# Optimization experiments

Hardware: AMD Instinct MI355X
Metric: run time of the kernel (lower is better)

The kernel has to match this reference:

```python
import jax, jax.numpy as jnp
import numpy as np

N_BANK = 1_000_000
D = 256
EPS = 1e-12  # torch F.normalize eps


def setup_inputs() -> dict:
    key = jax.random.key(0)
    k1, k2 = jax.random.split(key)
    query_emb = jax.random.normal(k1, (1, D), dtype=jnp.float32)
    emb_norm = jax.random.normal(k2, (N_BANK, D), dtype=jnp.float32)
    return {"query_emb": query_emb, "emb_norm": emb_norm, "k": 5}


def reference(query_emb, emb_norm, k):
    # L2-normalize query along feature dim (torch F.normalize semantics)
    norm = jnp.linalg.norm(query_emb, axis=1, keepdims=True)
    query = query_emb / jnp.maximum(norm, EPS)
    # [1, d] @ [d, N] -> [1, N] -> [N]
    sims = jnp.squeeze(query @ emb_norm.T, axis=0)
    top_vals, top_idx = jax.lax.top_k(sims, k)
    return (top_idx, top_vals)
```

## Files before the change

### kernel.cpp

```cpp
#include <hip/hip_runtime.h>
#include <cfloat>
#include <math.h>


#define D 256
#define TPB 256
#define NBLOCKS 1024
#define WAVES_PER_BLOCK (TPB / 64)
#define NWAVES (NBLOCKS * WAVES_PER_BLOCK)
#define KSEL 5

__device__ __forceinline__ float wave_sum(float v) {
    #pragma unroll
    for (int o = 32; o > 0; o >>= 1) v += __shfl_xor(v, o, 64);
    return v;
}

__device__ __forceinline__ void top5_insert(float (&bv)[KSEL], int (&bi)[KSEL],
                                            float d, int row) {
    if (d > bv[KSEL - 1]) {
        int j = KSEL - 1;
        while (j > 0 && d > bv[j - 1]) {
            bv[j] = bv[j - 1]; bi[j] = bi[j - 1]; --j;
        }
        bv[j] = d; bi[j] = row;
    }
}

__global__ __launch_bounds__(TPB) void knn_dots(
        const float* __restrict__ q, const float* __restrict__ bank, int n,
        float* __restrict__ cand_val, int* __restrict__ cand_idx) {
    const int lane = threadIdx.x & 63;
    const int wave = (blockIdx.x * TPB + threadIdx.x) >> 6;

    const float4 q4 = reinterpret_cast<const float4*>(q)[lane];

    const int rpw   = (n + NWAVES - 1) / NWAVES;
    const int start = wave * rpw;
    const int end   = min(start + rpw, n);

    float bv[KSEL]; int bi[KSEL];
    #pragma unroll
    for (int j = 0; j < KSEL; ++j) { bv[j] = -FLT_MAX; bi[j] = 0; }

    int row = start;
    for (; row + 4 <= end; row += 4) {
        const float4* r0 = reinterpret_cast<const float4*>(bank + (size_t)(row + 0) * D);
        const float4* r1 = reinterpret_cast<const float4*>(bank + (size_t)(row + 1) * D);
        const float4* r2 = reinterpret_cast<const float4*>(bank + (size_t)(row + 2) * D);
        const float4* r3 = reinterpret_cast<const float4*>(bank + (size_t)(row + 3) * D);
        float4 a0 = r0[lane], a1 = r1[lane], a2 = r2[lane], a3 = r3[lane];

        float d0 = a0.x * q4.x + a0.y * q4.y + a0.z * q4.z + a0.w * q4.w;
        float d1 = a1.x * q4.x + a1.y * q4.y + a1.z * q4.z + a1.w * q4.w;
        float d2 = a2.x * q4.x + a2.y * q4.y + a2.z * q4.z + a2.w * q4.w;
        float d3 = a3.x * q4.x + a3.y * q4.y + a3.z * q4.z + a3.w * q4.w;

        #pragma unroll
        for (int o = 32; o > 0; o >>= 1) {
            d0 += __shfl_xor(d0, o, 64);
            d1 += __shfl_xor(d1, o, 64);
            d2 += __shfl_xor(d2, o, 64);
            d3 += __shfl_xor(d3, o, 64);
        }

        top5_insert(bv, bi, d0, row + 0);
        top5_insert(bv, bi, d1, row + 1);
        top5_insert(bv, bi, d2, row + 2);
        top5_insert(bv, bi, d3, row + 3);
    }
    for (; row < end; ++row) {
        const float4* r = reinterpret_cast<const float4*>(bank + (size_t)row * D);
        float4 a = r[lane];
        float d = a.x * q4.x + a.y * q4.y + a.z * q4.z + a.w * q4.w;
        d = wave_sum(d);
        top5_insert(bv, bi, d, row);
    }

    if (lane == 0) {
        #pragma unroll
        for (int j = 0; j < KSEL; ++j) {
            cand_val[wave * KSEL + j] = bv[j];
            cand_idx[wave * KSEL + j] = bi[j];
        }
    }
}

__global__ __launch_bounds__(TPB) void knn_select(
        const float* __restrict__ q,
        const float* __restrict__ cand_val, const int* __restrict__ cand_idx,
        float* __restrict__ out) {
    __shared__ float svals[TPB];
    __shared__ int   sidx[TPB];
    __shared__ int   spos[TPB];
    __shared__ int   selpos[KSEL];
    __shared__ int   selidx[KSEL];
    __shared__ float selval[KSEL];
    __shared__ float snorm;

    const int t = threadIdx.x;

    float x = q[t];
    svals[t] = x * x;
    __syncthreads();
    for (int s = 128; s > 0; s >>= 1) {
        if (t < s) svals[t] += svals[t + s];
        __syncthreads();
    }
    if (t == 0) snorm = sqrtf(svals[0]);
    __syncthreads();

    const int C = NWAVES * KSEL;
    for (int r = 0; r < KSEL; ++r) {
        float best = -FLT_MAX; int bidx = 0x7fffffff; int bpos = -1;
        for (int p = t; p < C; p += TPB) {
            bool skip = false;
            for (int j = 0; j < r; ++j) skip |= (selpos[j] == p);
            if (skip) continue;
            float v = cand_val[p];
            int  ix = cand_idx[p];
            if (v > best || (v == best && ix < bidx)) { best = v; bidx = ix; bpos = p; }
        }
        svals[t] = best; sidx[t] = bidx; spos[t] = bpos;
        __syncthreads();
        for (int s = 128; s > 0; s >>= 1) {
            if (t < s) {
                bool take = (svals[t + s] > svals[t]) ||
                            (svals[t + s] == svals[t] && sidx[t + s] < sidx[t]);
                if (take) { svals[t] = svals[t + s]; sidx[t] = sidx[t + s]; spos[t] = spos[t + s]; }
            }
            __syncthreads();
        }
        if (t == 0) { selpos[r] = spos[0]; selidx[r] = sidx[0]; selval[r] = svals[0]; }
        __syncthreads();
    }

    if (t == 0) {
        float inv = 1.0f / fmaxf(snorm, 1e-12f);
        #pragma unroll
        for (int j = 0; j < KSEL; ++j) {
            out[j]        = (float)selidx[j];
            out[KSEL + j] = selval[j] * inv;
        }
    }
}

extern "C" void kernel_launch(void* const* d_in, const int* in_sizes, int n_in,
                              void* d_out, int out_size, void* d_ws, size_t ws_size,
                              hipStream_t stream) {
    const float* q    = (const float*)d_in[0];
    const float* bank = (const float*)d_in[1];
    const int n = in_sizes[1] / D;

    float* cand_val = (float*)d_ws;
    int*   cand_idx = (int*)(cand_val + NWAVES * KSEL);
    float* out = (float*)d_out;

    knn_dots<<<NBLOCKS, TPB, 0, stream>>>(q, bank, n, cand_val, cand_idx);
    knn_select<<<1, TPB, 0, stream>>>(q, cand_val, cand_idx, out);
}
```

Baseline: 1.397 ms.

## Interleave wave reductions, double block count, single-pass top-k select

In the dot kernel, the four per-row wave reductions are interleaved: lanes swap partial sums at the first two shuffle stages, so only one value is fully reduced and the four sums are then broadcast. This replaces 24 shuffles with about 10. The block count doubles so more waves stream the bank. The select kernel changes from five serial argmax passes over all candidates to one pass that keeps a per-thread top-5, followed by a shared-memory and shuffle merge. This cuts the serial tail work, but the larger candidate count adds input to the select stage.

Measured after the change: 1.369 ms. 2.0% less time.

```diff
diff --git a/kernel.cpp b/kernel.cpp
--- a/kernel.cpp
+++ b/kernel.cpp
@@ -1,14 +1,15 @@
 #include <hip/hip_runtime.h>
 #include <cfloat>
+#include <limits.h>
 #include <math.h>
 
 
 #define D 256
 #define TPB 256
-#define NBLOCKS 1024
-#define WAVES_PER_BLOCK (TPB / 64)
-#define NWAVES (NBLOCKS * WAVES_PER_BLOCK)
+#define NBLOCKS 2048
+#define NWAVES (NBLOCKS * (TPB / 64))
 #define KSEL 5
+#define NCAND (NWAVES * KSEL)
 
 __device__ __forceinline__ float wave_sum(float v) {
     #pragma unroll
@@ -34,6 +35,7 @@
     const int wave = (blockIdx.x * TPB + threadIdx.x) >> 6;
 
     const float4 q4 = reinterpret_cast<const float4*>(q)[lane];
+    const float4* __restrict__ b4 = reinterpret_cast<const float4*>(bank);
 
     const int rpw   = (n + NWAVES - 1) / NWAVES;
     const int start = wave * rpw;
@@ -45,34 +47,42 @@
 
     int row = start;
     for (; row + 4 <= end; row += 4) {
-        const float4* r0 = reinterpret_cast<const float4*>(bank + (size_t)(row + 0) * D);
-        const float4* r1 = reinterpret_cast<const float4*>(bank + (size_t)(row + 1) * D);
-        const float4* r2 = reinterpret_cast<const float4*>(bank + (size_t)(row + 2) * D);
-        const float4* r3 = reinterpret_cast<const float4*>(bank + (size_t)(row + 3) * D);
-        float4 a0 = r0[lane], a1 = r1[lane], a2 = r2[lane], a3 = r3[lane];
+        const float4* base = b4 + (size_t)row * (D / 4) + lane;
+        float4 a0 = base[0];
+        float4 a1 = base[64];
+        float4 a2 = base[128];
+        float4 a3 = base[192];
 
-        float d0 = a0.x * q4.x + a0.y * q4.y + a0.z * q4.z + a0.w * q4.w;
-        float d1 = a1.x * q4.x + a1.y * q4.y + a1.z * q4.z + a1.w * q4.w;
-        float d2 = a2.x * q4.x + a2.y * q4.y + a2.z * q4.z + a2.w * q4.w;
-        float d3 = a3.x * q4.x + a3.y * q4.y + a3.z * q4.z + a3.w * q4.w;
+        float d0 = fmaf(a0.x, q4.x, fmaf(a0.y, q4.y, fmaf(a0.z, q4.z, a0.w * q4.w)));
+        float d1 = fmaf(a1.x, q4.x, fmaf(a1.y, q4.y, fmaf(a1.z, q4.z, a1.w * q4.w)));
+        float d2 = fmaf(a2.x, q4.x, fmaf(a2.y, q4.y, fmaf(a2.z, q4.z, a2.w * q4.w)));
+        float d3 = fmaf(a3.x, q4.x, fmaf(a3.y, q4.y, fmaf(a3.z, q4.z, a3.w * q4.w)));
 
+        d0 += __shfl_xor(d0, 32, 64);
+        d1 += __shfl_xor(d1, 32, 64);
+        d2 += __shfl_xor(d2, 32, 64);
+        d3 += __shfl_xor(d3, 32, 64);
+        float e01 = (lane & 32) ? d1 : d0;
+        float e23 = (lane & 32) ? d3 : d2;
+        e01 += __shfl_xor(e01, 16, 64);
+        e23 += __shfl_xor(e23, 16, 64);
+        float f = (lane & 16) ? e23 : e01;
         #pragma unroll
-        for (int o = 32; o > 0; o >>= 1) {
-            d0 += __shfl_xor(d0, o, 64);
-            d1 += __shfl_xor(d1, o, 64);
-            d2 += __shfl_xor(d2, o, 64);
-            d3 += __shfl_xor(d3, o, 64);
-        }
+        for (int o = 8; o > 0; o >>= 1) f += __shfl_xor(f, o, 64);
 
-        top5_insert(bv, bi, d0, row + 0);
-        top5_insert(bv, bi, d1, row + 1);
-        top5_insert(bv, bi, d2, row + 2);
-        top5_insert(bv, bi, d3, row + 3);
+        float s0 = __shfl(f, 0, 64);
+        float s2 = __shfl(f, 16, 64);
+        float s1 = __shfl(f, 32, 64);
+        float s3 = __shfl(f, 48, 64);
+
+        top5_insert(bv, bi, s0, row + 0);
+        top5_insert(bv, bi, s1, row + 1);
+        top5_insert(bv, bi, s2, row + 2);
+        top5_insert(bv, bi, s3, row + 3);
     }
     for (; row < end; ++row) {
-        const float4* r = reinterpret_cast<const float4*>(bank + (size_t)row * D);
-        float4 a = r[lane];
-        float d = a.x * q4.x + a.y * q4.y + a.z * q4.z + a.w * q4.w;
+        float4 a = b4[(size_t)row * (D / 4) + lane];
+        float d = fmaf(a.x, q4.x, fmaf(a.y, q4.y, fmaf(a.z, q4.z, a.w * q4.w)));
         d = wave_sum(d);
         top5_insert(bv, bi, d, row);
     }
@@ -86,61 +96,79 @@
     }
 }
 
+__device__ __forceinline__ bool better(float v, int ix, float bv, int bi) {
+    return (v > bv) || (v == bv && ix < bi);
+}
+
+__device__ __forceinline__ void top5_insert_ti(float (&bv)[KSEL], int (&bi)[KSEL],
+                                               float v, int ix) {
+    if (better(v, ix, bv[KSEL - 1], bi[KSEL - 1])) {
+        int j = KSEL - 1;
+        while (j > 0 && better(v, ix, bv[j - 1], bi[j - 1])) {
+            bv[j] = bv[j - 1]; bi[j] = bi[j - 1]; --j;
+        }
+        bv[j] = v; bi[j] = ix;
+    }
+}
+
 __global__ __launch_bounds__(TPB) void knn_select(
         const float* __restrict__ q,
         const float* __restrict__ cand_val, const int* __restrict__ cand_idx,
         float* __restrict__ out) {
-    __shared__ float svals[TPB];
-    __shared__ int   sidx[TPB];
-    __shared__ int   spos[TPB];
-    __shared__ int   selpos[KSEL];
-    __shared__ int   selidx[KSEL];
-    __shared__ float selval[KSEL];
-    __shared__ float snorm;
+    __shared__ float lv[TPB * KSEL];
+    __shared__ int   li[TPB * KSEL];
+    __shared__ float wsum[TPB / 64];
 
     const int t = threadIdx.x;
+    const int lane = t & 63;
 
     float x = q[t];
-    svals[t] = x * x;
-    __syncthreads();
-    for (int s = 128; s > 0; s >>= 1) {
-        if (t < s) svals[t] += svals[t + s];
-        __syncthreads();
+    float xx = x * x;
+    #pragma unroll
+    for (int o = 32; o > 0; o >>= 1) xx += __shfl_xor(xx, o, 64);
+    if (lane == 0) wsum[t >> 6] = xx;
+
+    float bv[KSEL]; int bi[KSEL];
+    #pragma unroll
+    for (int j = 0; j < KSEL; ++j) { bv[j] = -FLT_MAX; bi[j] = INT_MAX; }
+    for (int p = t; p < NCAND; p += TPB) {
+        float v = cand_val[p];
+        int  ix = cand_idx[p];
+        top5_insert_ti(bv, bi, v, ix);
     }
-    if (t == 0) snorm = sqrtf(svals[0]);
+    #pragma unroll
+    for (int j = 0; j < KSEL; ++j) { lv[t * KSEL + j] = bv[j]; li[t * KSEL + j] = bi[j]; }
     __syncthreads();
 
-    const int C = NWAVES * KSEL;
-    for (int r = 0; r < KSEL; ++r) {
-        float best = -FLT_MAX; int bidx = 0x7fffffff; int bpos = -1;
-        for (int p = t; p < C; p += TPB) {
-            bool skip = false;
-            for (int j = 0; j < r; ++j) skip |= (selpos[j] == p);
-            if (skip) continue;
-            float v = cand_val[p];
-            int  ix = cand_idx[p];
-            if (v > best || (v == best && ix < bidx)) { best = v; bidx = ix; bpos = p; }
+    if (t < 64) {
+        #pragma unroll
+        for (int j = 0; j < KSEL; ++j) { bv[j] = -FLT_MAX; bi[j] = INT_MAX; }
+        const int base = t * 4 * KSEL;
+        for (int p = 0; p < 4 * KSEL; ++p)
+            top5_insert_ti(bv, bi, lv[base + p], li[base + p]);
+
+        #pragma unroll
+        for (int o = 32; o > 0; o >>= 1) {
+            float ov[KSEL]; int oi[KSEL];
+            #pragma unroll
+            for (int j = 0; j < KSEL; ++j) {
+                ov[j] = __shfl_down(bv[j], o, 64);
+                oi[j] = __shfl_down(bi[j], o, 64);
+            }
+            if (t < o) {
+                #pragma unroll
+                for (int j = 0; j < KSEL; ++j) top5_insert_ti(bv, bi, ov[j], oi[j]);
+            }
         }
-        svals[t] = best; sidx[t] = bidx; spos[t] = bpos;
-        __syncthreads();
-        for (int s = 128; s > 0; s >>= 1) {
-            if (t < s) {
-                bool take = (svals[t + s] > svals[t]) ||
-                            (svals[t + s] == svals[t] && sidx[t + s] < sidx[t]);
-                if (take) { svals[t] = svals[t + s]; sidx[t] = sidx[t + s]; spos[t] = spos[t + s]; }
+
+        if (t == 0) {
+            float nrm = sqrtf(wsum[0] + wsum[1] + wsum[2] + wsum[3]);
+            float inv = 1.0f / fmaxf(nrm, 1e-12f);
+            #pragma unroll
+            for (int j = 0; j < KSEL; ++j) {
+                out[j]        = (float)bi[j];
+                out[KSEL + j] = bv[j] * inv;
             }
-            __syncthreads();
-        }
-        if (t == 0) { selpos[r] = spos[0]; selidx[r] = sidx[0]; selval[r] = svals[0]; }
-        __syncthreads();
-    }
-
-    if (t == 0) {
-        float inv = 1.0f / fmaxf(snorm, 1e-12f);
-        #pragma unroll
-        for (int j = 0; j < KSEL; ++j) {
-            out[j]        = (float)selidx[j];
-            out[KSEL + j] = selval[j] * inv;
         }
     }
 }
@@ -153,7 +181,7 @@
     const int n = in_sizes[1] / D;
 
     float* cand_val = (float*)d_ws;
-    int*   cand_idx = (int*)(cand_val + NWAVES * KSEL);
+    int*   cand_idx = (int*)(cand_val + NCAND);
     float* out = (float*)d_out;
 
     knn_dots<<<NBLOCKS, TPB, 0, stream>>>(q, bank, n, cand_val, cand_idx);
```
